# Kernel tuning notes

Hardware: AMD Instinct MI355X
Metric: run time of the kernel (lower is better)

## Reference

```python
import jax, jax.numpy as jnp
import numpy as np

N_NODES = 100000
N_EDGES = 600000
IN_DIM = 128
HID = 128
OUT_CH = 64
NUM_LAYERS = 3  # plus one final GINConv -> 4 conv layers total


def setup_inputs() -> dict:
    key = jax.random.key(0)
    ks = jax.random.split(key, 16)
    x = jax.random.normal(ks[0], (N_NODES, IN_DIM), dtype=jnp.float32)
    src = jax.random.randint(ks[1], (N_EDGES,), 0, N_NODES, dtype=jnp.int32)
    dst = jax.random.randint(ks[2], (N_EDGES,), 0, N_NODES, dtype=jnp.int32)
    s = 0.05
    # First NUM_LAYERS GINConv layers all map 128->128 (stacked), final maps 128->64->64.
    w1s = jax.random.normal(ks[3], (NUM_LAYERS, IN_DIM, HID), dtype=jnp.float32) * s
    b1s = jnp.zeros((NUM_LAYERS, HID), dtype=jnp.float32)
    w2s = jax.random.normal(ks[4], (NUM_LAYERS, HID, HID), dtype=jnp.float32) * s
    b2s = jnp.zeros((NUM_LAYERS, HID), dtype=jnp.float32)
    wf1 = jax.random.normal(ks[5], (HID, OUT_CH), dtype=jnp.float32) * s
    bf1 = jnp.zeros((OUT_CH,), dtype=jnp.float32)
    wf2 = jax.random.normal(ks[6], (OUT_CH, OUT_CH), dtype=jnp.float32) * s
    bf2 = jnp.zeros((OUT_CH,), dtype=jnp.float32)
    eps = jnp.zeros((NUM_LAYERS + 1,), dtype=jnp.float32)  # DGL GINConv learn_eps init 0
    return {"x": x, "src": src, "dst": dst, "eps": eps,
            "w1s": w1s, "b1s": b1s, "w2s": w2s, "b2s": b2s,
            "wf1": wf1, "bf1": bf1, "wf2": wf2, "bf2": bf2}


def _gin_conv(h, src, dst, eps, w1, b1, w2, b2):
    # mean aggregation over incoming edges (scatter-mean by dst of src features)
    n = h.shape[0]
    neigh_sum = jax.ops.segment_sum(h[src], dst, num_segments=n)
    deg = jax.ops.segment_sum(jnp.ones(src.shape[0], h.dtype), dst, num_segments=n)
    mean_neigh = neigh_sum / jnp.maximum(deg, 1.0)[:, None]
    z = (1.0 + eps) * h + mean_neigh
    # 2-layer MLP (Dropout inactive at eval): Linear -> LeakyReLU -> Linear -> LeakyReLU
    z = jax.nn.leaky_relu(z @ w1 + b1)
    return jax.nn.leaky_relu(z @ w2 + b2)


def reference(x, src, dst, eps, w1s, b1s, w2s, b2s, wf1, bf1, wf2, bf2):
    h = x
    for l in range(NUM_LAYERS):
        h = _gin_conv(h, src, dst, eps[l], w1s[l], b1s[l], w2s[l], b2s[l])
    h = _gin_conv(h, src, dst, eps[NUM_LAYERS], wf1, bf1, wf2, bf2)
    return h  # norm=False so no final L2 normalize
```

## Files before the change

kernel.cpp:

```cpp
#include <hip/hip_runtime.h>
#include <hip/hip_fp16.h>

#define NCH 128

typedef short bf16x8 __attribute__((ext_vector_type(8)));
typedef float f32x4 __attribute__((ext_vector_type(4)));

__device__ __forceinline__ unsigned short f32_to_bf16_rne(float f) {
    unsigned u = __float_as_uint(f);
    unsigned r = u + 0x7FFFu + ((u >> 16) & 1u);
    return (unsigned short)(r >> 16);
}
__device__ __forceinline__ void split_bf16(float f, unsigned short& hi, unsigned short& lo) {
    unsigned u = __float_as_uint(f);
    hi = (unsigned short)(u >> 16);
    float l = f - __uint_as_float(u & 0xFFFF0000u);
    lo = f32_to_bf16_rne(l);
}


__global__ void gin_deg_kernel(const int* __restrict__ dst, int* __restrict__ off, int E) {
    int e = blockIdx.x * 256 + threadIdx.x;
    if (e < E) atomicAdd(&off[dst[e] + 1], 1);
}

__global__ void gin_scan1(const int* __restrict__ off, int* __restrict__ part,
                          int* __restrict__ hist, int n) {
    __shared__ int red[256];
    __shared__ int lh[64];
    int t = threadIdx.x;
    if (t < 64) lh[t] = 0;
    __syncthreads();
    int base = blockIdx.x * 2048 + t * 8;
    int s = 0;
    for (int i = 0; i < 8; ++i) {
        int idx = base + i;
        if (idx < n) {
            int v = off[idx];
            s += v;
            if (idx > 0) atomicAdd(&lh[min(v, 63)], 1);
        }
    }
    red[t] = s;
    __syncthreads();
    #pragma unroll
    for (int o = 128; o > 0; o >>= 1) {
        if (t < o) red[t] += red[t + o];
        __syncthreads();
    }
    if (t == 0) part[blockIdx.x] = red[0];
    if (t < 64 && lh[t]) atomicAdd(&hist[t], lh[t]);
}

__global__ void gin_scan2(int* __restrict__ part, int nb) {
    __shared__ int sh[256];
    int t = threadIdx.x;
    int v = (t < nb) ? part[t] : 0;
    sh[t] = v;
    __syncthreads();
    #pragma unroll
    for (int o = 1; o < 256; o <<= 1) {
        int u = (t >= o) ? sh[t - o] : 0;
        __syncthreads();
        sh[t] += u;
        __syncthreads();
    }
    if (t < nb) part[t] = sh[t] - v;
}

__global__ void gin_scan3(int* __restrict__ off, const int* __restrict__ part, int n) {
    __shared__ int red[256];
    int t = threadIdx.x;
    int base = blockIdx.x * 2048 + t * 8;
    int loc[8];
    int s = 0;
    #pragma unroll
    for (int i = 0; i < 8; ++i) {
        int idx = base + i;
        int v = (idx < n) ? off[idx] : 0;
        s += v;
        loc[i] = s;
    }
    red[t] = s;
    __syncthreads();
    #pragma unroll
    for (int o = 1; o < 256; o <<= 1) {
        int u = (t >= o) ? red[t - o] : 0;
        __syncthreads();
        red[t] += u;
        __syncthreads();
    }
    int offset = part[blockIdx.x] + red[t] - s;
    #pragma unroll
    for (int i = 0; i < 8; ++i) {
        int idx = base + i;
        if (idx < n) off[idx] = loc[i] + offset;
    }
}

__global__ void gin_fill_kernel(const int* __restrict__ src, const int* __restrict__ dst,
                                int* __restrict__ off, int* __restrict__ csr, int E) {
    int e = blockIdx.x * 256 + threadIdx.x;
    if (e < E) {
        int d = dst[e];
        int p = atomicAdd(&off[d], 1);
        csr[p] = src[e];
    }
}

__global__ void gin_binbase_kernel(const int* __restrict__ hist, int* __restrict__ cursor) {
    int t = threadIdx.x;
    int v = hist[t];
    int s = v;
    #pragma unroll
    for (int o = 1; o < 64; o <<= 1) {
        int u = __shfl_up(s, o, 64);
        if (t >= o) s += u;
    }
    int total = __shfl(s, 63, 64);
    cursor[t] = total - s;
}

__global__ void gin_permfill_kernel(const int* __restrict__ offend, int* __restrict__ cursor,
                                    int* __restrict__ perm, int n) {
    __shared__ int lh[64];
    __shared__ int lbase[64];
    int t = threadIdx.x;
    if (t < 64) lh[t] = 0;
    __syncthreads();
    int i = blockIdx.x * 256 + t;
    int d = 0, rank = 0;
    if (i < n) {
        d = min(offend[i] - (i ? offend[i - 1] : 0), 63);
        rank = atomicAdd(&lh[d], 1);
    }
    __syncthreads();
    if (t < 64 && lh[t]) lbase[t] = atomicAdd(&cursor[t], lh[t]);
    __syncthreads();
    if (i < n) perm[lbase[d] + rank] = i;
}

__global__ void gin_f2h_kernel(const float* __restrict__ x, __half* __restrict__ xh, int n4) {
    int i = blockIdx.x * 256 + threadIdx.x;
    if (i >= n4) return;
    float4 v = ((const float4*)x)[i];
    union { __half h[4]; uint2 u; } o;
    o.h[0] = __float2half(v.x); o.h[1] = __float2half(v.y);
    o.h[2] = __float2half(v.z); o.h[3] = __float2half(v.w);
    ((uint2*)xh)[i] = o.u;
}

__global__ void gin_packall_kernel(const float* __restrict__ w1s, const float* __restrict__ w2s,
                                   const float* __restrict__ wf1, const float* __restrict__ wf2,
                                   unsigned short* __restrict__ pw1, unsigned short* __restrict__ pw2,
                                   unsigned short* __restrict__ pwf1, unsigned short* __restrict__ pwf2) {
    int idx = blockIdx.x * 256 + threadIdx.x;
    const float* W; unsigned short* out; int K, N, e;
    if (idx < 98304) {
        int layer = idx >> 15; e = idx & 32767;
        W = w1s + (size_t)layer * 16384; out = pw1 + (size_t)layer * 32768; K = 128; N = 128;
    } else if (idx < 196608) {
        int j = idx - 98304; int layer = j >> 15; e = j & 32767;
        W = w2s + (size_t)layer * 16384; out = pw2 + (size_t)layer * 32768; K = 128; N = 128;
    } else if (idx < 212992) {
        e = idx - 196608; W = wf1; out = pwf1; K = 128; N = 64;
    } else if (idx < 221184) {
        e = idx - 212992; W = wf2; out = pwf2; K = 64; N = 64;
    } else return;
    int KC = K / 32, NT = N / 16;
    int j = e & 7;
    int l = (e >> 3) & 63;
    int v = e >> 9;
    int nt = v % NT; v /= NT;
    int kc = v % KC;
    int spl = v / KC;
    int k = kc * 32 + (l >> 4) * 8 + j;
    int n = nt * 16 + (l & 15);
    float w = W[(size_t)k * N + n];
    unsigned short hi, lo;
    split_bf16(w, hi, lo);
    out[e] = (spl == 0) ? hi : lo;
}

template <int N1, int N2, typename OutT>
__global__ __launch_bounds__(256, 4)
void gin_fused(const __half* __restrict__ Hin, const int* __restrict__ offend,
               const int* __restrict__ csr, const int* __restrict__ perm,
               const float* __restrict__ eps_p, int layer,
               const unsigned short* __restrict__ PW1, const float* __restrict__ B1,
               const unsigned short* __restrict__ PW2, const float* __restrict__ B2,
               OutT* __restrict__ Out, int nrows) {
    constexpr int K1 = 128;
    constexpr int KC1 = K1 / 32, NT1 = N1 / 16, KC2 = N1 / 32, NT2 = N2 / 16;
    constexpr int SS = 36;
    __shared__ __align__(16) float Scr[4 * 16 * SS];

    const int tid = threadIdx.x;
    const int w = tid >> 6;
    const int l = tid & 63;
    const int lr = l & 15;
    const int lg = l >> 4;
    const int m0 = blockIdx.x * 64 + w * 16;
    const int slot = m0 + lr;
    float* sw = &Scr[w * 16 * SS];

    union { bf16x8 v; unsigned short u[8]; } AH[KC1], AL[KC1];

    if (slot < nrows) {
        const int node = perm[slot];
        int lo = node ? offend[node - 1] : 0;
        int hi = offend[node];
        float s[KC1][8];
        #pragma unroll
        for (int kc = 0; kc < KC1; ++kc)
            #pragma unroll
            for (int j = 0; j < 8; ++j) s[kc][j] = 0.f;

        const size_t coff = (size_t)lg * 8;
        int e = lo;
        const int him1 = hi - 1;
        int i0 = 0, i1 = 0, i2 = 0, i3 = 0;
        if (e < hi) {
            i0 = csr[min(e,     him1)];
            i1 = csr[min(e + 1, him1)];
            i2 = csr[min(e + 2, him1)];
            i3 = csr[min(e + 3, him1)];
        }
        while (e + 3 < hi) {
            int c0 = i0, c1 = i1, c2 = i2, c3 = i3;
            e += 4;
            i0 = csr[min(e,     him1)];
            i1 = csr[min(e + 1, him1)];
            i2 = csr[min(e + 2, him1)];
            i3 = csr[min(e + 3, him1)];
            const uint4* p0 = (const uint4*)(Hin + (size_t)c0 * NCH + coff);
            const uint4* p1 = (const uint4*)(Hin + (size_t)c1 * NCH + coff);
            const uint4* p2 = (const uint4*)(Hin + (size_t)c2 * NCH + coff);
            const uint4* p3 = (const uint4*)(Hin + (size_t)c3 * NCH + coff);
            uint4 r0[KC1], r1[KC1], r2[KC1], r3[KC1];
            #pragma unroll
            for (int kc = 0; kc < KC1; ++kc) {
                r0[kc] = p0[kc * 4]; r1[kc] = p1[kc * 4];
                r2[kc] = p2[kc * 4]; r3[kc] = p3[kc * 4];
            }
            #pragma unroll
            for (int kc = 0; kc < KC1; ++kc) {
                const __half2* h0 = (const __half2*)&r0[kc];
                const __half2* h1 = (const __half2*)&r1[kc];
                const __half2* h2 = (const __half2*)&r2[kc];
                const __half2* h3 = (const __half2*)&r3[kc];
                #pragma unroll
                for (int j = 0; j < 4; ++j) {
                    float2 f0 = __half22float2(h0[j]);
                    float2 f1 = __half22float2(h1[j]);
                    float2 f2 = __half22float2(h2[j]);
                    float2 f3 = __half22float2(h3[j]);
                    s[kc][j * 2]     += (f0.x + f1.x) + (f2.x + f3.x);
                    s[kc][j * 2 + 1] += (f0.y + f1.y) + (f2.y + f3.y);
                }
            }
        }
        for (; e + 1 < hi; e += 2) {
            int a0 = csr[e], a1 = csr[e + 1];
            const uint4* p0 = (const uint4*)(Hin + (size_t)a0 * NCH + coff);
            const uint4* p1 = (const uint4*)(Hin + (size_t)a1 * NCH + coff);
            uint4 r0[KC1], r1[KC1];
            #pragma unroll
            for (int kc = 0; kc < KC1; ++kc) { r0[kc] = p0[kc * 4]; r1[kc] = p1[kc * 4]; }
            #pragma unroll
            for (int kc = 0; kc < KC1; ++kc) {
                const __half2* h0 = (const __half2*)&r0[kc];
                const __half2* h1 = (const __half2*)&r1[kc];
                #pragma unroll
                for (int j = 0; j < 4; ++j) {
                    float2 f0 = __half22float2(h0[j]);
                    float2 f1 = __half22float2(h1[j]);
                    s[kc][j * 2]     += f0.x + f1.x;
                    s[kc][j * 2 + 1] += f0.y + f1.y;
                }
            }
        }
        if (e < hi) {
            const uint4* p0 = (const uint4*)(Hin + (size_t)csr[e] * NCH + coff);
            uint4 r0[KC1];
            #pragma unroll
            for (int kc = 0; kc < KC1; ++kc) r0[kc] = p0[kc * 4];
            #pragma unroll
            for (int kc = 0; kc < KC1; ++kc) {
                const __half2* h0 = (const __half2*)&r0[kc];
                #pragma unroll
                for (int j = 0; j < 4; ++j) {
                    float2 f0 = __half22float2(h0[j]);
                    s[kc][j * 2]     += f0.x;
                    s[kc][j * 2 + 1] += f0.y;
                }
            }
        }
        float invd = 1.0f / fmaxf((float)(hi - lo), 1.0f);
        float e1 = 1.0f + eps_p[layer];
        const uint4* ps = (const uint4*)(Hin + (size_t)node * NCH + coff);
        #pragma unroll
        for (int kc = 0; kc < KC1; ++kc) {
            uint4 rs = ps[kc * 4];
            const __half2* hs = (const __half2*)&rs;
            #pragma unroll
            for (int j = 0; j < 4; ++j) {
                float2 fs = __half22float2(hs[j]);
                float z0 = e1 * fs.x + s[kc][j * 2] * invd;
                float z1 = e1 * fs.y + s[kc][j * 2 + 1] * invd;
                split_bf16(z0, AH[kc].u[j * 2], AL[kc].u[j * 2]);
                split_bf16(z1, AH[kc].u[j * 2 + 1], AL[kc].u[j * 2 + 1]);
            }
        }
    } else {
        #pragma unroll
        for (int kc = 0; kc < KC1; ++kc) {
            AH[kc].v = (bf16x8){0,0,0,0,0,0,0,0};
            AL[kc].v = (bf16x8){0,0,0,0,0,0,0,0};
        }
    }

    f32x4 acc[NT1];
    #pragma unroll
    for (int nt = 0; nt < NT1; ++nt) acc[nt] = {0.f, 0.f, 0.f, 0.f};

    #pragma unroll
    for (int kc = 0; kc < KC1; ++kc) {
        #pragma unroll
        for (int nt = 0; nt < NT1; ++nt) {
            const unsigned short* pb = PW1 + (((size_t)kc * NT1 + nt) * 64 + l) * 8;
            bf16x8 bh = *(const bf16x8*)pb;
            bf16x8 bl = *(const bf16x8*)(pb + (size_t)KC1 * NT1 * 512);
            acc[nt] = __builtin_amdgcn_mfma_f32_16x16x32_bf16(AH[kc].v, bh, acc[nt], 0, 0, 0);
            acc[nt] = __builtin_amdgcn_mfma_f32_16x16x32_bf16(AH[kc].v, bl, acc[nt], 0, 0, 0);
            acc[nt] = __builtin_amdgcn_mfma_f32_16x16x32_bf16(AL[kc].v, bh, acc[nt], 0, 0, 0);
        }
    }

    f32x4 acc2[NT2];
    #pragma unroll
    for (int nt = 0; nt < NT2; ++nt) acc2[nt] = {0.f, 0.f, 0.f, 0.f};

    #pragma unroll
    for (int kc = 0; kc < KC2; ++kc) {
        #pragma unroll
        for (int t = 0; t < 2; ++t) {
            int nt = kc * 2 + t;
            float bb = B1[nt * 16 + lr];
            #pragma unroll
            for (int r = 0; r < 4; ++r) {
                float v = acc[nt][r] + bb;
                v = v > 0.f ? v : 0.01f * v;
                sw[(lg * 4 + r) * SS + t * 16 + lr] = v;
            }
        }
        const float* tp = &sw[lr * SS + lg * 8];
        f32x4 v0 = *(const f32x4*)tp;
        f32x4 v1 = *(const f32x4*)(tp + 4);
        union { bf16x8 v; unsigned short u[8]; } H, L;
        #pragma unroll
        for (int i = 0; i < 4; ++i) {
            split_bf16(v0[i], H.u[i], L.u[i]);
            split_bf16(v1[i], H.u[i + 4], L.u[i + 4]);
        }
        bf16x8 ah = H.v, al = L.v;
        #pragma unroll
        for (int nt = 0; nt < NT2; ++nt) {
            const unsigned short* pb = PW2 + (((size_t)kc * NT2 + nt) * 64 + l) * 8;
            bf16x8 bh = *(const bf16x8*)pb;
            bf16x8 bl = *(const bf16x8*)(pb + (size_t)KC2 * NT2 * 512);
            acc2[nt] = __builtin_amdgcn_mfma_f32_16x16x32_bf16(ah, bh, acc2[nt], 0, 0, 0);
            acc2[nt] = __builtin_amdgcn_mfma_f32_16x16x32_bf16(ah, bl, acc2[nt], 0, 0, 0);
            acc2[nt] = __builtin_amdgcn_mfma_f32_16x16x32_bf16(al, bh, acc2[nt], 0, 0, 0);
        }
    }

    int onode[4];
    #pragma unroll
    for (int r = 0; r < 4; ++r) {
        int s2 = m0 + lg * 4 + r;
        onode[r] = (s2 < nrows) ? perm[s2] : -1;
    }
    #pragma unroll
    for (int nt = 0; nt < NT2; ++nt) {
        float bb = B2[nt * 16 + lr];
        #pragma unroll
        for (int r = 0; r < 4; ++r) {
            if (onode[r] >= 0) {
                float v = acc2[nt][r] + bb;
                v = v > 0.f ? v : 0.01f * v;
                Out[(size_t)onode[r] * N2 + nt * 16 + lr] = (OutT)v;
            }
        }
    }
}


extern "C" void kernel_launch(void* const* d_in, const int* in_sizes, int n_in,
                              void* d_out, int out_size, void* d_ws, size_t ws_size,
                              hipStream_t stream) {
    const float* x   = (const float*)d_in[0];
    const int*   src = (const int*)d_in[1];
    const int*   dst = (const int*)d_in[2];
    const float* eps = (const float*)d_in[3];
    const float* w1s = (const float*)d_in[4];
    const float* b1s = (const float*)d_in[5];
    const float* w2s = (const float*)d_in[6];
    const float* b2s = (const float*)d_in[7];
    const float* wf1 = (const float*)d_in[8];
    const float* bf1 = (const float*)d_in[9];
    const float* wf2 = (const float*)d_in[10];
    const float* bf2 = (const float*)d_in[11];

    const int N = in_sizes[0] / NCH;
    const int E = in_sizes[1];

    auto align256 = [](size_t v) { return (v + 255) & ~(size_t)255; };
    char* p = (char*)d_ws;
    int* off = (int*)p;              p += align256((size_t)(N + 1) * 4);
    int* hist = (int*)p;             p += align256(64 * 4);
    int* part = (int*)p;             p += align256(1024 * 4);
    int* cursor = (int*)p;           p += align256(64 * 4);
    int* perm = (int*)p;             p += align256((size_t)N * 4);
    int* csr = (int*)p;              p += align256((size_t)E * 4);
    __half* xh = (__half*)p;         p += align256((size_t)N * NCH * 2);
    __half* h0 = (__half*)p;         p += align256((size_t)N * NCH * 2);
    __half* h1 = (__half*)p;         p += align256((size_t)N * NCH * 2);
    unsigned short* pw1 = (unsigned short*)p; p += 3 * 65536;
    unsigned short* pw2 = (unsigned short*)p; p += 3 * 65536;
    unsigned short* pwf1 = (unsigned short*)p; p += 32768;
    unsigned short* pwf2 = (unsigned short*)p;

    const int nScan = N + 1;
    const int nTiles = (nScan + 2047) / 2048;
    hipMemsetAsync(off, 0, align256((size_t)nScan * 4) + 64 * 4, stream);

    gin_deg_kernel<<<(E + 255) / 256, 256, 0, stream>>>(dst, off, E);
    gin_scan1<<<nTiles, 256, 0, stream>>>(off, part, hist, nScan);
    gin_scan2<<<1, 256, 0, stream>>>(part, nTiles);
    gin_scan3<<<nTiles, 256, 0, stream>>>(off, part, nScan);
    gin_fill_kernel<<<(E + 255) / 256, 256, 0, stream>>>(src, dst, off, csr, E);

    gin_binbase_kernel<<<1, 64, 0, stream>>>(hist, cursor);
    gin_permfill_kernel<<<(N + 255) / 256, 256, 0, stream>>>(off, cursor, perm, N);

    const int n4 = N * NCH / 4;
    gin_f2h_kernel<<<(n4 + 255) / 256, 256, 0, stream>>>(x, xh, n4);

    gin_packall_kernel<<<(221184 + 255) / 256, 256, 0, stream>>>(
        w1s, w2s, wf1, wf2, pw1, pw2, pwf1, pwf2);

    const int grid = (N + 63) / 64;

    gin_fused<128, 128, __half><<<grid, 256, 0, stream>>>(
        xh, off, csr, perm, eps, 0, pw1, b1s, pw2, b2s, h0, N);
    gin_fused<128, 128, __half><<<grid, 256, 0, stream>>>(
        h0, off, csr, perm, eps, 1, pw1 + 32768, b1s + 128, pw2 + 32768, b2s + 128, h1, N);
    gin_fused<128, 128, __half><<<grid, 256, 0, stream>>>(
        h1, off, csr, perm, eps, 2, pw1 + 65536, b1s + 256, pw2 + 65536, b2s + 256, h0, N);
    gin_fused<64, 64, float><<<grid, 256, 0, stream>>>(
        h0, off, csr, perm, eps, 3, pwf1, bf1, pwf2, bf2, (float*)d_out, N);
}
```

Baseline: 342.5 us.

## Split neighbor gather across helper waves with LDS partial-sum reduction

Doubles the block to 512 threads. Four extra helper waves each take the second half of their row's edge list, then hand their partial sums to the main waves through shared memory in two halves before the helpers exit. The aim is more memory-level parallelism in the latency-bound gather and a shorter per-row critical path. In exchange it adds three block barriers and extra LDS, and 512-thread blocks with launch_bounds(512,4) may squeeze registers or occupancy.

Result: slower. 400.3 us (+16.9%).

```diff
diff --git a/kernel.cpp b/kernel.cpp
--- a/kernel.cpp
+++ b/kernel.cpp
@@ -183,7 +183,7 @@
 }
 
 template <int N1, int N2, typename OutT>
-__global__ __launch_bounds__(256, 4)
+__global__ __launch_bounds__(512, 4)
 void gin_fused(const __half* __restrict__ Hin, const int* __restrict__ offend,
                const int* __restrict__ csr, const int* __restrict__ perm,
                const float* __restrict__ eps_p, int layer,
@@ -193,112 +193,150 @@
     constexpr int K1 = 128;
     constexpr int KC1 = K1 / 32, NT1 = N1 / 16, KC2 = N1 / 32, NT2 = N2 / 16;
     constexpr int SS = 36;
+    constexpr int PS = 68;
     __shared__ __align__(16) float Scr[4 * 16 * SS];
+    __shared__ __align__(16) float Part[4 * 16 * PS];
 
     const int tid = threadIdx.x;
     const int w = tid >> 6;
+    const bool helper = w >= 4;
+    const int wv = w & 3;
     const int l = tid & 63;
     const int lr = l & 15;
     const int lg = l >> 4;
-    const int m0 = blockIdx.x * 64 + w * 16;
+    const int m0 = blockIdx.x * 64 + wv * 16;
     const int slot = m0 + lr;
-    float* sw = &Scr[w * 16 * SS];
-
-    union { bf16x8 v; unsigned short u[8]; } AH[KC1], AL[KC1];
-
+    float* sw = &Scr[wv * 16 * SS];
+    float* pp = &Part[(wv * 16 + lr) * PS];
+
+    float s[KC1][8];
+    #pragma unroll
+    for (int kc = 0; kc < KC1; ++kc)
+        #pragma unroll
+        for (int j = 0; j < 8; ++j) s[kc][j] = 0.f;
+
+    int lo = 0, hi = 0, node = -1;
     if (slot < nrows) {
-        const int node = perm[slot];
-        int lo = node ? offend[node - 1] : 0;
-        int hi = offend[node];
-        float s[KC1][8];
-        #pragma unroll
-        for (int kc = 0; kc < KC1; ++kc)
-            #pragma unroll
-            for (int j = 0; j < 8; ++j) s[kc][j] = 0.f;
+        node = perm[slot];
+        lo = node ? offend[node - 1] : 0;
+        hi = offend[node];
+        int mid = lo + (((hi - lo) + 1) >> 1);
+        int b  = helper ? mid : lo;
+        int e2 = helper ? hi  : mid;
 
         const size_t coff = (size_t)lg * 8;
-        int e = lo;
-        const int him1 = hi - 1;
-        int i0 = 0, i1 = 0, i2 = 0, i3 = 0;
-        if (e < hi) {
-            i0 = csr[min(e,     him1)];
-            i1 = csr[min(e + 1, him1)];
-            i2 = csr[min(e + 2, him1)];
-            i3 = csr[min(e + 3, him1)];
-        }
-        while (e + 3 < hi) {
-            int c0 = i0, c1 = i1, c2 = i2, c3 = i3;
-            e += 4;
-            i0 = csr[min(e,     him1)];
-            i1 = csr[min(e + 1, him1)];
-            i2 = csr[min(e + 2, him1)];
-            i3 = csr[min(e + 3, him1)];
-            const uint4* p0 = (const uint4*)(Hin + (size_t)c0 * NCH + coff);
-            const uint4* p1 = (const uint4*)(Hin + (size_t)c1 * NCH + coff);
-            const uint4* p2 = (const uint4*)(Hin + (size_t)c2 * NCH + coff);
-            const uint4* p3 = (const uint4*)(Hin + (size_t)c3 * NCH + coff);
-            uint4 r0[KC1], r1[KC1], r2[KC1], r3[KC1];
-            #pragma unroll
-            for (int kc = 0; kc < KC1; ++kc) {
-                r0[kc] = p0[kc * 4]; r1[kc] = p1[kc * 4];
-                r2[kc] = p2[kc * 4]; r3[kc] = p3[kc * 4];
-            }
-            #pragma unroll
-            for (int kc = 0; kc < KC1; ++kc) {
-                const __half2* h0 = (const __half2*)&r0[kc];
-                const __half2* h1 = (const __half2*)&r1[kc];
-                const __half2* h2 = (const __half2*)&r2[kc];
-                const __half2* h3 = (const __half2*)&r3[kc];
+        if (b < e2) {
+            int e = b;
+            const int em1 = e2 - 1;
+            int i0 = csr[min(e,     em1)];
+            int i1 = csr[min(e + 1, em1)];
+            int i2 = csr[min(e + 2, em1)];
+            int i3 = csr[min(e + 3, em1)];
+            while (e + 3 < e2) {
+                int c0 = i0, c1 = i1, c2 = i2, c3 = i3;
+                e += 4;
+                i0 = csr[min(e,     em1)];
+                i1 = csr[min(e + 1, em1)];
+                i2 = csr[min(e + 2, em1)];
+                i3 = csr[min(e + 3, em1)];
+                const uint4* p0 = (const uint4*)(Hin + (size_t)c0 * NCH + coff);
+                const uint4* p1 = (const uint4*)(Hin + (size_t)c1 * NCH + coff);
+                const uint4* p2 = (const uint4*)(Hin + (size_t)c2 * NCH + coff);
+                const uint4* p3 = (const uint4*)(Hin + (size_t)c3 * NCH + coff);
+                uint4 r0[KC1], r1[KC1], r2[KC1], r3[KC1];
                 #pragma unroll
-                for (int j = 0; j < 4; ++j) {
-                    float2 f0 = __half22float2(h0[j]);
-                    float2 f1 = __half22float2(h1[j]);
-                    float2 f2 = __half22float2(h2[j]);
-                    float2 f3 = __half22float2(h3[j]);
-                    s[kc][j * 2]     += (f0.x + f1.x) + (f2.x + f3.x);
-                    s[kc][j * 2 + 1] += (f0.y + f1.y) + (f2.y + f3.y);
+                for (int kc = 0; kc < KC1; ++kc) {
+                    r0[kc] = p0[kc * 4]; r1[kc] = p1[kc * 4];
+                    r2[kc] = p2[kc * 4]; r3[kc] = p3[kc * 4];
+                }
+                #pragma unroll
+                for (int kc = 0; kc < KC1; ++kc) {
+                    const __half2* h0 = (const __half2*)&r0[kc];
+                    const __half2* h1 = (const __half2*)&r1[kc];
+                    const __half2* h2 = (const __half2*)&r2[kc];
+                    const __half2* h3 = (const __half2*)&r3[kc];
+                    #pragma unroll
+                    for (int j = 0; j < 4; ++j) {
+                        float2 f0 = __half22float2(h0[j]);
+                        float2 f1 = __half22float2(h1[j]);
+                        float2 f2 = __half22float2(h2[j]);
+                        float2 f3 = __half22float2(h3[j]);
+                        s[kc][j * 2]     += (f0.x + f1.x) + (f2.x + f3.x);
+                        s[kc][j * 2 + 1] += (f0.y + f1.y) + (f2.y + f3.y);
+                    }
                 }
             }
-        }
-        for (; e + 1 < hi; e += 2) {
-            int a0 = csr[e], a1 = csr[e + 1];
-            const uint4* p0 = (const uint4*)(Hin + (size_t)a0 * NCH + coff);
-            const uint4* p1 = (const uint4*)(Hin + (size_t)a1 * NCH + coff);
-            uint4 r0[KC1], r1[KC1];
-            #pragma unroll
-            for (int kc = 0; kc < KC1; ++kc) { r0[kc] = p0[kc * 4]; r1[kc] = p1[kc * 4]; }
-            #pragma unroll
-            for (int kc = 0; kc < KC1; ++kc) {
-                const __half2* h0 = (const __half2*)&r0[kc];
-                const __half2* h1 = (const __half2*)&r1[kc];
+            for (; e + 1 < e2; e += 2) {
+                int a0 = csr[e], a1 = csr[e + 1];
+                const uint4* p0 = (const uint4*)(Hin + (size_t)a0 * NCH + coff);
+                const uint4* p1 = (const uint4*)(Hin + (size_t)a1 * NCH + coff);
+                uint4 r0[KC1], r1[KC1];
                 #pragma unroll
-                for (int j = 0; j < 4; ++j) {
-                    float2 f0 = __half22float2(h0[j]);
-                    float2 f1 = __half22float2(h1[j]);
-                    s[kc][j * 2]     += f0.x + f1.x;
-                    s[kc][j * 2 + 1] += f0.y + f1.y;
+                for (int kc = 0; kc < KC1; ++kc) { r0[kc] = p0[kc * 4]; r1[kc] = p1[kc * 4]; }
+                #pragma unroll
+                for (int kc = 0; kc < KC1; ++kc) {
+                    const __half2* h0 = (const __half2*)&r0[kc];
+                    const __half2* h1 = (const __half2*)&r1[kc];
+                    #pragma unroll
+                    for (int j = 0; j < 4; ++j) {
+                        float2 f0 = __half22float2(h0[j]);
+                        float2 f1 = __half22float2(h1[j]);
+                        s[kc][j * 2]     += f0.x + f1.x;
+                        s[kc][j * 2 + 1] += f0.y + f1.y;
+                    }
                 }
             }
-        }
-        if (e < hi) {
-            const uint4* p0 = (const uint4*)(Hin + (size_t)csr[e] * NCH + coff);
-            uint4 r0[KC1];
-            #pragma unroll
-            for (int kc = 0; kc < KC1; ++kc) r0[kc] = p0[kc * 4];
-            #pragma unroll
-            for (int kc = 0; kc < KC1; ++kc) {
-                const __half2* h0 = (const __half2*)&r0[kc];
+            if (e < e2) {
+                const uint4* p0 = (const uint4*)(Hin + (size_t)csr[e] * NCH + coff);
+                uint4 r0[KC1];
                 #pragma unroll
-                for (int j = 0; j < 4; ++j) {
-                    float2 f0 = __half22float2(h0[j]);
-                    s[kc][j * 2]     += f0.x;
-                    s[kc][j * 2 + 1] += f0.y;
+                for (int kc = 0; kc < KC1; ++kc) r0[kc] = p0[kc * 4];
+                #pragma unroll
+                for (int kc = 0; kc < KC1; ++kc) {
+                    const __half2* h0 = (const __half2*)&r0[kc];
+                    #pragma unroll
+                    for (int j = 0; j < 4; ++j) {
+                        float2 f0 = __half22float2(h0[j]);
+                        s[kc][j * 2]     += f0.x;
+                        s[kc][j * 2 + 1] += f0.y;
+                    }
                 }
             }
         }
+    }
+
+    if (helper) {
+        #pragma unroll
+        for (int kc = 0; kc < 2; ++kc)
+            #pragma unroll
+            for (int j = 0; j < 8; ++j) pp[kc * 32 + lg * 8 + j] = s[kc][j];
+    }
+    __syncthreads();
+    if (!helper) {
+        #pragma unroll
+        for (int kc = 0; kc < 2; ++kc)
+            #pragma unroll
+            for (int j = 0; j < 8; ++j) s[kc][j] += pp[kc * 32 + lg * 8 + j];
+    }
+    __syncthreads();
+    if (helper) {
+        #pragma unroll
+        for (int kc = 2; kc < 4; ++kc)
+            #pragma unroll
+            for (int j = 0; j < 8; ++j) pp[(kc - 2) * 32 + lg * 8 + j] = s[kc][j];
+    }
+    __syncthreads();
+    if (helper) return;
+    #pragma unroll
+    for (int kc = 2; kc < 4; ++kc)
+        #pragma unroll
+        for (int j = 0; j < 8; ++j) s[kc][j] += pp[(kc - 2) * 32 + lg * 8 + j];
+
+    union { bf16x8 v; unsigned short u[8]; } AH[KC1], AL[KC1];
+    if (slot < nrows) {
         float invd = 1.0f / fmaxf((float)(hi - lo), 1.0f);
         float e1 = 1.0f + eps_p[layer];
-        const uint4* ps = (const uint4*)(Hin + (size_t)node * NCH + coff);
+        const uint4* ps = (const uint4*)(Hin + (size_t)node * NCH + (size_t)lg * 8);
         #pragma unroll
         for (int kc = 0; kc < KC1; ++kc) {
             uint4 rs = ps[kc * 4];
@@ -452,12 +490,12 @@
 
     const int grid = (N + 63) / 64;
 
-    gin_fused<128, 128, __half><<<grid, 256, 0, stream>>>(
+    gin_fused<128, 128, __half><<<grid, 512, 0, stream>>>(
         xh, off, csr, perm, eps, 0, pw1, b1s, pw2, b2s, h0, N);
-    gin_fused<128, 128, __half><<<grid, 256, 0, stream>>>(
+    gin_fused<128, 128, __half><<<grid, 512, 0, stream>>>(
         h0, off, csr, perm, eps, 1, pw1 + 32768, b1s + 128, pw2 + 32768, b2s + 128, h1, N);
-    gin_fused<128, 128, __half><<<grid, 256, 0, stream>>>(
+    gin_fused<128, 128, __half><<<grid, 512, 0, stream>>>(
         h1, off, csr, perm, eps, 2, pw1 + 65536, b1s + 256, pw2 + 65536, b2s + 256, h0, N);
-    gin_fused<64, 64, float><<<grid, 256, 0, stream>>>(
+    gin_fused<64, 64, float><<<grid, 512, 0, stream>>>(
         h0, off, csr, perm, eps, 3, pwf1, bf1, pwf2, bf2, (float*)d_out, N);
 }
```
